# Kernel optimization log

Measured on AMD Instinct MI355X. Metric: run time of the kernel, lower is better.

## Reference

```python
import jax, jax.numpy as jnp
import numpy as np

L, H, D, DH, DFF = 6, 8, 512, 64, 2048
EPS = 1e-5


def setup_inputs() -> dict:
    key = jax.random.key(0)
    ks = jax.random.split(key, 20)
    B, S, T = 16, 512, 512
    s = 0.02
    inp = {
        "x": jax.random.normal(ks[0], (B, S, D), jnp.float32),
        "y": jax.random.normal(ks[1], (B, T, D), jnp.float32),
        # self-attention per-head projections, stacked over layers and heads
        "Wq1": jax.random.normal(ks[2], (L, H, D, DH), jnp.float32) * s,
        "Wk1": jax.random.normal(ks[3], (L, H, D, DH), jnp.float32) * s,
        "Wv1": jax.random.normal(ks[4], (L, H, D, DH), jnp.float32) * s,
        "Wo1": jax.random.normal(ks[5], (L, D, D), jnp.float32) * s,
        # cross-attention
        "Wq2": jax.random.normal(ks[6], (L, H, D, DH), jnp.float32) * s,
        "Wk2": jax.random.normal(ks[7], (L, H, D, DH), jnp.float32) * s,
        "Wv2": jax.random.normal(ks[8], (L, H, D, DH), jnp.float32) * s,
        "Wo2": jax.random.normal(ks[9], (L, D, D), jnp.float32) * s,
        # position-wise FFN
        "W1": jax.random.normal(ks[10], (L, D, DFF), jnp.float32) * s,
        "bf1": jnp.zeros((L, DFF), jnp.float32),
        "W2": jax.random.normal(ks[11], (L, DFF, D), jnp.float32) * s,
        "bf2": jnp.zeros((L, D), jnp.float32),
        # layer norms
        "ln1_g": jnp.ones((L, D), jnp.float32), "ln1_b": jnp.zeros((L, D), jnp.float32),
        "ln2_g": jnp.ones((L, D), jnp.float32), "ln2_b": jnp.zeros((L, D), jnp.float32),
        "ln3_g": jnp.ones((L, D), jnp.float32), "ln3_b": jnp.zeros((L, D), jnp.float32),
    }
    return inp


def _layer_norm(x, g, b):
    m = jnp.mean(x, axis=-1, keepdims=True)
    v = jnp.mean(jnp.square(x - m), axis=-1, keepdims=True)
    return (x - m) * jax.lax.rsqrt(v + EPS) * g + b


def _mha(q_in, kv_in, Wq, Wk, Wv, Wo, causal):
    # Wq/Wk/Wv: [H, D, DH]; batched equivalent of the per-head Linear loop
    q = jnp.einsum("bsd,hdk->bhsk", q_in, Wq)
    k = jnp.einsum("btd,hdk->bhtk", kv_in, Wk)
    v = jnp.einsum("btd,hdk->bhtk", kv_in, Wv)
    scores = jnp.einsum("bhsk,bhtk->bhst", q, k) / jnp.sqrt(jnp.float32(DH))
    if causal:
        S, T = scores.shape[-2], scores.shape[-1]
        mask = jnp.tril(jnp.ones((S, T), bool))
        scores = jnp.where(mask, scores, -jnp.inf)
    p = jax.nn.softmax(scores, axis=-1)
    out = jnp.einsum("bhst,bhtk->bhsk", p, v)
    B, _, S, _ = out.shape
    out = out.transpose(0, 2, 1, 3).reshape(B, S, H * DH)  # concat heads (dim=2 order)
    return out @ Wo


def reference(x, y, Wq1, Wk1, Wv1, Wo1, Wq2, Wk2, Wv2, Wo2,
              W1, bf1, W2, bf2, ln1_g, ln1_b, ln2_g, ln2_b, ln3_g, ln3_b):
    for l in range(L):
        # masked self-attention + residual + LN  (dropout = identity in eval)
        a1 = _mha(x, x, Wq1[l], Wk1[l], Wv1[l], Wo1[l], causal=True)
        h1 = _layer_norm(a1 + x, ln1_g[l], ln1_b[l])
        # cross-attention (queries from decoder, K/V from encoder output y)
        a2 = _mha(h1, y, Wq2[l], Wk2[l], Wv2[l], Wo2[l], causal=False)
        h2 = _layer_norm(a2 + h1, ln2_g[l], ln2_b[l])
        # position-wise FFN (batched over all positions)
        f = jax.nn.relu(h2 @ W1[l] + bf1[l]) @ W2[l] + bf2[l]
        x = _layer_norm(f + h2, ln3_g[l], ln3_b[l])
    return x
```

## Files before the change

kernel.cpp:

```cpp
#include <hip/hip_runtime.h>

typedef __bf16 bf16;
typedef __attribute__((ext_vector_type(8))) __bf16 bf16x8;
typedef __attribute__((ext_vector_type(4))) __bf16 bf16x4;
typedef __attribute__((ext_vector_type(4))) float f32x4;

#define GL16(gp, lp) __builtin_amdgcn_global_load_lds( \
    (const __attribute__((address_space(1))) unsigned int*)(gp), \
    (__attribute__((address_space(3))) unsigned int*)(lp), 16, 0, 0)

__device__ __forceinline__ f32x4 mfma16(bf16x8 a, bf16x8 b, f32x4 c) {
  return __builtin_amdgcn_mfma_f32_16x16x32_bf16(a, b, c, 0, 0, 0);
}

template<int BN, int RELU, int BIAS, int RES, int OUTB, int VTO>
__global__ __launch_bounds__(256, (BN == 64) ? 3 : 2) void gemm_k(
    const bf16* __restrict__ A, const bf16* __restrict__ Bt,
    float* __restrict__ Cf, bf16* __restrict__ Cb,
    const float* __restrict__ bias, const bf16* __restrict__ resid,
    bf16* __restrict__ vt, int vtc0,
    int M, int N, int ldc, int K)
{
  constexpr int MI = 4;
  constexpr int NI = BN / 32;
  __shared__ __align__(16) bf16 smem[(2 * 128 + 2 * BN) * 64];
  bf16* Al0 = smem;
  bf16* Bl0 = smem + 2 * 128 * 64;
  const int tid = threadIdx.x;
  const int wid = tid >> 6, lane = tid & 63;
  const int g = lane >> 4, l16 = lane & 15;

  const int lin = blockIdx.x + gridDim.x * blockIdx.y;
  const int nwg = gridDim.x * gridDim.y;
  int bx, by;
  if ((nwg & 7) == 0 && gridDim.y == 64 && gridDim.x >= 16) {
    const int xcd = lin & 7, c = lin >> 3;
    by = (xcd << 3) + (c & 7);
    bx = c >> 3;
  } else if ((nwg & 7) == 0) {
    const int l2 = (lin & 7) * (nwg >> 3) + (lin >> 3);
    bx = l2 % gridDim.x; by = l2 / gridDim.x;
  } else {
    bx = lin % gridDim.x; by = lin / gridDim.x;
  }

  const int bm = by * 128, bn = bx * BN;
  const int wm = (wid >> 1) * 64;
  const int wn = (wid & 1) * (BN / 2);

  const f32x4 z4 = {0.f, 0.f, 0.f, 0.f};
  f32x4 acc[MI][NI];
#pragma unroll
  for (int i = 0; i < MI; ++i)
#pragma unroll
    for (int j = 0; j < NI; ++j) acc[i][j] = z4;

  const int sr = tid >> 3;
  const int scs = ((((tid & 7) * 16) ^ ((sr & 7) << 4)) >> 1);
  const bf16* Ag = A + (size_t)(bm + sr) * K + scs;
  const bf16* Bg = Bt + (size_t)(bn + sr) * K + scs;
  const size_t kstep32 = (size_t)32 * K;

  auto stage = [&](int sel, int k0) {
#pragma unroll
    for (int sw = 0; sw < 4; ++sw)
      GL16(Ag + k0 + sw * kstep32, &Al0[sel * 8192 + sw * 2048 + tid * 8]);
#pragma unroll
    for (int sw = 0; sw < BN / 32; ++sw)
      GL16(Bg + k0 + sw * kstep32, &Bl0[sel * (BN * 64) + sw * 2048 + tid * 8]);
  };

  const int nsteps = K >> 6;
  stage(0, 0);
  int cur = 0;
  for (int s = 0; s < nsteps; ++s) {
    __builtin_amdgcn_sched_barrier(0);
    asm volatile("s_waitcnt vmcnt(0)" ::: "memory");
    __builtin_amdgcn_s_barrier();
    __builtin_amdgcn_sched_barrier(0);
    if (s + 1 < nsteps) stage(cur ^ 1, (s + 1) * 64);
    bf16x8 af[MI][2], bfr[NI][2];
#pragma unroll
    for (int mi = 0; mi < MI; ++mi) {
      const int row = wm + mi * 16 + l16;
      const int rs = (row & 7) << 4;
#pragma unroll
      for (int kh = 0; kh < 2; ++kh)
        af[mi][kh] = *(const bf16x8*)&Al0[cur * 8192 + row * 64 + (((g * 16 + kh * 64) ^ rs) >> 1)];
    }
#pragma unroll
    for (int ni = 0; ni < NI; ++ni) {
      const int row = wn + ni * 16 + l16;
      const int rs = (row & 7) << 4;
#pragma unroll
      for (int kh = 0; kh < 2; ++kh)
        bfr[ni][kh] = *(const bf16x8*)&Bl0[cur * (BN * 64) + row * 64 + (((g * 16 + kh * 64) ^ rs) >> 1)];
    }
#pragma unroll
    for (int kh = 0; kh < 2; ++kh)
#pragma unroll
      for (int mi = 0; mi < MI; ++mi)
#pragma unroll
        for (int ni = 0; ni < NI; ++ni)
          acc[mi][ni] = mfma16(af[mi][kh], bfr[ni][kh], acc[mi][ni]);
    cur ^= 1;
  }

  if (VTO && bn >= vtc0) {
    __syncthreads();
    bf16* stg = smem;
#pragma unroll
    for (int mi = 0; mi < MI; ++mi) {
#pragma unroll
      for (int ni = 0; ni < NI; ++ni) {
        const int dhl = wn + ni * 16 + l16;
        const int t0 = wm + mi * 16 + g * 4;
        bf16x4 v4;
#pragma unroll
        for (int r = 0; r < 4; ++r) v4[r] = (bf16)acc[mi][ni][r];
        *(bf16x4*)&stg[dhl * 136 + t0] = v4;
      }
    }
    __syncthreads();
    const int b0 = bm >> 9, tseg = bm & 511;
#pragma unroll
    for (int it = 0; it < BN / 16; ++it) {
      const int flat = it * 256 + tid;
      const int dhl = flat >> 4;
      const int t8 = (flat & 15) * 8;
      const int gdh = bn + dhl - vtc0;
      const int lL = gdh >> 9, hh = (gdh >> 6) & 7, dh = gdh & 63;
      const bf16x8 v = *(const bf16x8*)&stg[dhl * 136 + t8];
      *(bf16x8*)&vt[(((size_t)lL * 128 + b0 * 8 + hh) * 64 + dh) * 512 + tseg + t8] = v;
    }
    return;
  }

#pragma unroll
  for (int mi = 0; mi < MI; ++mi) {
#pragma unroll
    for (int ni = 0; ni < NI; ++ni) {
#pragma unroll
      for (int r = 0; r < 4; ++r) {
        const int row = bm + wm + mi * 16 + g * 4 + r;
        const int col = bn + wn + ni * 16 + l16;
        float v = acc[mi][ni][r];
        if (BIAS) v += bias[col];
        const size_t idx = (size_t)row * ldc + col;
        if (RES)  v += (float)resid[idx];
        if (RELU) v = fmaxf(v, 0.f);
        if (OUTB) Cb[idx] = (bf16)v;
        else      Cf[idx] = v;
      }
    }
  }
}

template<int CAUSAL>
__global__ __launch_bounds__(256, 4) void attn_k(
    const bf16* __restrict__ Q, const bf16* __restrict__ Kg,
    const bf16* __restrict__ VT, bf16* __restrict__ O, int qs, int kvs)
{
  __shared__ __align__(16) bf16 Kl[2][64 * 64];
  __shared__ __align__(16) bf16 Vl[2][64 * 64];
  __shared__ __align__(16) bf16 plb[4 * 16 * 64];
  const int tid = threadIdx.x;
  const int wid = tid >> 6, lane = tid & 63;
  const int g = lane >> 4, l16 = lane & 15;

  int lin = blockIdx.x + 8 * blockIdx.y + 64 * blockIdx.z;
  lin = (lin & 7) * 128 + (lin >> 3);
  const int qt = lin & 7, h = (lin >> 3) & 7, b = lin >> 6;

  const int q0 = qt * 64 + wid * 16;
  const size_t tokQ = (size_t)b * 512 + q0;

  const bf16* qp = Q + (tokQ + l16) * (size_t)qs + h * 64 + g * 8;
  const bf16x8 qf0 = *(const bf16x8*)qp;
  const bf16x8 qf1 = *(const bf16x8*)(qp + 32);

  const int sr = tid >> 3;
  const int cs2 = ((((tid & 7) * 16) ^ ((sr & 7) << 4)) >> 1);
  const bf16* Ksrc = Kg + ((size_t)b * 512 + sr) * kvs + h * 64 + cs2;
  const bf16* Vsrc = VT + (size_t)(b * 8 + h) * 64 * 512 + (size_t)sr * 512 + cs2;
  bf16* pw = plb + wid * 1024;

  auto stage = [&](int sel, int t0) {
    GL16(Ksrc + (size_t)t0 * kvs, &Kl[sel][tid * 8]);
    GL16(Ksrc + (size_t)(t0 + 32) * kvs, &Kl[sel][tid * 8 + 2048]);
    GL16(Vsrc + t0, &Vl[sel][tid * 8]);
    GL16(Vsrc + 32 * 512 + t0, &Vl[sel][tid * 8 + 2048]);
  };

  const f32x4 z4 = {0.f, 0.f, 0.f, 0.f};
  float m[4], ls[4];
  f32x4 o[4];
#pragma unroll
  for (int r = 0; r < 4; ++r) { m[r] = -1e30f; ls[r] = 0.f; o[r] = z4; }

  const int sw = (l16 & 7) << 4;
  const int ktmax = CAUSAL ? qt : 7;
  stage(0, 0);
  int cur = 0;
  for (int kt = 0; kt <= ktmax; ++kt) {
    const int t0 = kt * 64;
    __builtin_amdgcn_sched_barrier(0);
    asm volatile("s_waitcnt vmcnt(0)" ::: "memory");
    __builtin_amdgcn_s_barrier();
    if (kt < ktmax) stage(cur ^ 1, t0 + 64);

    f32x4 sc[4];
#pragma unroll
    for (int jt = 0; jt < 4; ++jt) {
      const int rk = jt * 16 + l16;
      const bf16x8 kf0 = *(const bf16x8*)&Kl[cur][rk * 64 + (((g * 16) ^ sw) >> 1)];
      const bf16x8 kf1 = *(const bf16x8*)&Kl[cur][rk * 64 + (((g * 16 + 64) ^ sw) >> 1)];
      sc[jt] = mfma16(qf0, kf0, z4);
      sc[jt] = mfma16(qf1, kf1, sc[jt]);
    }
#pragma unroll
    for (int r = 0; r < 4; ++r) {
      const int q = g * 4 + r;
      const int srow = q0 + q;
      const int qs7 = (q & 7) << 4;
      float pv[4];
      float mx = -1e30f;
#pragma unroll
      for (int jt = 0; jt < 4; ++jt) {
        float v = sc[jt][r] * 0.125f;
        if (CAUSAL && (t0 + jt * 16 + l16) > srow) v = -1e30f;
        pv[jt] = v;
        mx = fmaxf(mx, v);
      }
#pragma unroll
      for (int msk = 8; msk; msk >>= 1) mx = fmaxf(mx, __shfl_xor(mx, msk));
      const float mn = fmaxf(m[r], mx);
      const float corr = __expf(m[r] - mn);
      float s = 0.f;
#pragma unroll
      for (int jt = 0; jt < 4; ++jt) {
        const float p = __expf(pv[jt] - mn);
        s += p;
        const int sb = (((jt * 16 + l16) * 2) ^ qs7) >> 1;
        pw[q * 64 + sb] = (bf16)p;
      }
#pragma unroll
      for (int msk = 8; msk; msk >>= 1) s += __shfl_xor(s, msk);
      ls[r] = ls[r] * corr + s;
      m[r] = mn;
#pragma unroll
      for (int j = 0; j < 4; ++j) o[j][r] *= corr;
    }
    asm volatile("s_waitcnt lgkmcnt(0)" ::: "memory");
    __builtin_amdgcn_sched_barrier(0);
    const bf16x8 pa0 = *(const bf16x8*)&pw[l16 * 64 + (((g * 16) ^ sw) >> 1)];
    const bf16x8 pa1 = *(const bf16x8*)&pw[l16 * 64 + (((g * 16 + 64) ^ sw) >> 1)];
#pragma unroll
    for (int j = 0; j < 4; ++j) {
      const int rv = j * 16 + l16;
      const bf16x8 vf0 = *(const bf16x8*)&Vl[cur][rv * 64 + (((g * 16) ^ sw) >> 1)];
      const bf16x8 vf1 = *(const bf16x8*)&Vl[cur][rv * 64 + (((g * 16 + 64) ^ sw) >> 1)];
      o[j] = mfma16(pa0, vf0, o[j]);
      o[j] = mfma16(pa1, vf1, o[j]);
    }
    cur ^= 1;
  }
#pragma unroll
  for (int r = 0; r < 4; ++r) {
    const float inv = 1.f / ls[r];
    bf16* op = O + (tokQ + g * 4 + r) * 512 + h * 64;
#pragma unroll
    for (int j = 0; j < 4; ++j) op[j * 16 + l16] = (bf16)(o[j][r] * inv);
  }
}

__global__ __launch_bounds__(256) void ln_k(
    const float* __restrict__ z, const float* __restrict__ gam,
    const float* __restrict__ bet, float* __restrict__ of,
    bf16* __restrict__ ob)
{
  const int wid = threadIdx.x >> 6, lane = threadIdx.x & 63;
  const int row = blockIdx.x * 4 + wid;
  const f32x4* zr = (const f32x4*)(z + (size_t)row * 512);
  const f32x4 a = zr[lane], c = zr[lane + 64];
  float s = 0.f, ss = 0.f;
#pragma unroll
  for (int e = 0; e < 4; ++e) {
    s += a[e] + c[e];
    ss += a[e] * a[e] + c[e] * c[e];
  }
#pragma unroll
  for (int msk = 32; msk; msk >>= 1) {
    s += __shfl_xor(s, msk);
    ss += __shfl_xor(ss, msk);
  }
  const float mean = s * (1.f / 512.f);
  const float var = ss * (1.f / 512.f) - mean * mean;
  const float rstd = rsqrtf(var + 1e-5f);
  const f32x4* gp = (const f32x4*)gam;
  const f32x4* bp = (const f32x4*)bet;
  const f32x4 g0 = gp[lane], g1 = gp[lane + 64];
  const f32x4 b0 = bp[lane], b1 = bp[lane + 64];
  f32x4 o0, o1;
#pragma unroll
  for (int e = 0; e < 4; ++e) {
    o0[e] = (a[e] - mean) * rstd * g0[e] + b0[e];
    o1[e] = (c[e] - mean) * rstd * g1[e] + b1[e];
  }
  if (of) {
    f32x4* ofr = (f32x4*)(of + (size_t)row * 512);
    ofr[lane] = o0;
    ofr[lane + 64] = o1;
  }
  if (ob) {
    bf16x4 c0, c1;
#pragma unroll
    for (int e = 0; e < 4; ++e) { c0[e] = (bf16)o0[e]; c1[e] = (bf16)o1[e]; }
    bf16x4* obr = (bf16x4*)(ob + (size_t)row * 512);
    obr[lane] = c0;
    obr[lane + 64] = c1;
  }
}

__global__ void transpose_cast(const float* __restrict__ src, bf16* __restrict__ dst,
                               int R, int C, int bpl, size_t lstride, size_t boff)
{
  __shared__ float t[32][33];
  const int z = blockIdx.z;
  src += (size_t)z * R * C;
  dst += (size_t)(z / bpl) * lstride + (size_t)(z % bpl) * ((size_t)R * C) + boff;
  const int c0 = blockIdx.x * 32, r0 = blockIdx.y * 32;
  const int tx = threadIdx.x, ty = threadIdx.y;
#pragma unroll
  for (int j = 0; j < 32; j += 8)
    t[ty + j][tx] = src[(size_t)(r0 + ty + j) * C + c0 + tx];
  __syncthreads();
#pragma unroll
  for (int j = 0; j < 32; j += 8)
    dst[(size_t)(c0 + ty + j) * R + r0 + tx] = (bf16)t[tx][ty + j];
}

__global__ void cast4(const float* __restrict__ s, bf16* __restrict__ d)
{
  const int i = blockIdx.x * 256 + threadIdx.x;
  const f32x4 v = ((const f32x4*)s)[i];
  bf16x4 c;
#pragma unroll
  for (int e = 0; e < 4; ++e) c[e] = (bf16)v[e];
  ((bf16x4*)d)[i] = c;
}

extern "C" void kernel_launch(void* const* d_in, const int* in_sizes, int n_in,
                              void* d_out, int out_size, void* d_ws, size_t ws_size,
                              hipStream_t stream)
{
  (void)in_sizes; (void)n_in; (void)out_size; (void)ws_size;
  const float* x   = (const float*)d_in[0];
  const float* y   = (const float*)d_in[1];
  const float* Wq1 = (const float*)d_in[2];
  const float* Wk1 = (const float*)d_in[3];
  const float* Wv1 = (const float*)d_in[4];
  const float* Wo1 = (const float*)d_in[5];
  const float* Wq2 = (const float*)d_in[6];
  const float* Wk2 = (const float*)d_in[7];
  const float* Wv2 = (const float*)d_in[8];
  const float* Wo2 = (const float*)d_in[9];
  const float* W1  = (const float*)d_in[10];
  const float* b1  = (const float*)d_in[11];
  const float* W2  = (const float*)d_in[12];
  const float* b2  = (const float*)d_in[13];
  const float* ln1g = (const float*)d_in[14];
  const float* ln1b = (const float*)d_in[15];
  const float* ln2g = (const float*)d_in[16];
  const float* ln2b = (const float*)d_in[17];
  const float* ln3g = (const float*)d_in[18];
  const float* ln3b = (const float*)d_in[19];

  char* ws = (char*)d_ws;
  size_t off = 0;
  auto alloc = [&](size_t bytes) -> void* {
    void* p = (void*)(ws + off);
    off += (bytes + 255) & ~(size_t)255;
    return p;
  };

  bf16* wqkv1t = (bf16*)alloc((size_t)6 * 1536 * 512 * 2);
  bf16* wo1t   = (bf16*)alloc((size_t)6 * 512 * 512 * 2);
  bf16* wq2t   = (bf16*)alloc((size_t)6 * 512 * 512 * 2);
  bf16* wkv2t  = (bf16*)alloc((size_t)6144 * 512 * 2);
  bf16* wo2t   = (bf16*)alloc((size_t)6 * 512 * 512 * 2);
  bf16* w1t    = (bf16*)alloc((size_t)6 * 512 * 2048 * 2);
  bf16* w2t    = (bf16*)alloc((size_t)6 * 2048 * 512 * 2);
  bf16* xb   = (bf16*)alloc((size_t)8192 * 512 * 2);
  bf16* yb   = (bf16*)alloc((size_t)8192 * 512 * 2);
  bf16* qkvb = (bf16*)alloc((size_t)8192 * 1536 * 2);
  bf16* qb   = (bf16*)alloc((size_t)8192 * 512 * 2);
  bf16* ab   = (bf16*)alloc((size_t)8192 * 512 * 2);
  bf16* h1b  = (bf16*)alloc((size_t)8192 * 512 * 2);
  bf16* h2b  = (bf16*)alloc((size_t)8192 * 512 * 2);
  float* zf  = (float*)alloc((size_t)8192 * 512 * 4);
  bf16* vt1  = (bf16*)alloc((size_t)8192 * 512 * 2);
  bf16* k2all  = (bf16*)alloc((size_t)8192 * 3072 * 2);
  bf16* vt2all = (bf16*)alloc((size_t)6 * 8192 * 512 * 2);
  bf16* f1b  = qkvb;

  const dim3 tb(32, 8);
  transpose_cast<<<dim3(2, 16, 48), tb, 0, stream>>>(Wq1, wqkv1t, 512, 64, 8, (size_t)1536 * 512, 0);
  transpose_cast<<<dim3(2, 16, 48), tb, 0, stream>>>(Wk1, wqkv1t, 512, 64, 8, (size_t)1536 * 512, (size_t)512 * 512);
  transpose_cast<<<dim3(2, 16, 48), tb, 0, stream>>>(Wv1, wqkv1t, 512, 64, 8, (size_t)1536 * 512, (size_t)1024 * 512);
  transpose_cast<<<dim3(16, 16, 6), tb, 0, stream>>>(Wo1, wo1t, 512, 512, 1, (size_t)512 * 512, 0);
  transpose_cast<<<dim3(2, 16, 48), tb, 0, stream>>>(Wq2, wq2t, 512, 64, 8, (size_t)512 * 512, 0);
  transpose_cast<<<dim3(2, 16, 48), tb, 0, stream>>>(Wk2, wkv2t, 512, 64, 8, (size_t)512 * 512, 0);
  transpose_cast<<<dim3(2, 16, 48), tb, 0, stream>>>(Wv2, wkv2t + (size_t)3072 * 512, 512, 64, 8, (size_t)512 * 512, 0);
  transpose_cast<<<dim3(16, 16, 6), tb, 0, stream>>>(Wo2, wo2t, 512, 512, 1, (size_t)512 * 512, 0);
  transpose_cast<<<dim3(64, 16, 6), tb, 0, stream>>>(W1, w1t, 512, 2048, 1, (size_t)512 * 2048, 0);
  transpose_cast<<<dim3(16, 64, 6), tb, 0, stream>>>(W2, w2t, 2048, 512, 1, (size_t)2048 * 512, 0);
  cast4<<<4096, 256, 0, stream>>>(x, xb);
  cast4<<<4096, 256, 0, stream>>>(y, yb);

  const dim3 g512s(8, 64), g1536(12, 64), gff(16, 64), g6144(48, 64);

  gemm_k<128, 0, 0, 0, 1, 1><<<g6144, 256, 0, stream>>>(yb, wkv2t, nullptr, k2all,
                                                        nullptr, nullptr, vt2all, 3072,
                                                        8192, 6144, 3072, 512);

  const bf16* curxb = xb;
  for (int l = 0; l < 6; ++l) {
    const bf16* WQKV1 = wqkv1t + (size_t)l * 1536 * 512;
    const bf16* WO1   = wo1t   + (size_t)l * 512 * 512;
    const bf16* WQ2   = wq2t   + (size_t)l * 512 * 512;
    const bf16* WO2   = wo2t   + (size_t)l * 512 * 512;
    const bf16* W1T   = w1t    + (size_t)l * 2048 * 512;
    const bf16* W2T   = w2t    + (size_t)l * 512 * 2048;

    gemm_k<128, 0, 0, 0, 1, 1><<<g1536, 256, 0, stream>>>(curxb, WQKV1, nullptr, qkvb,
                                                          nullptr, nullptr, vt1, 1024,
                                                          8192, 1536, 1536, 512);
    attn_k<1><<<dim3(8, 8, 16), 256, 0, stream>>>(qkvb, qkvb + 512, vt1, ab, 1536, 1536);
    gemm_k<64, 0, 0, 1, 0, 0><<<g512s, 256, 0, stream>>>(ab, WO1, zf, nullptr,
                                                         nullptr, curxb, nullptr, 0,
                                                         8192, 512, 512, 512);
    ln_k<<<2048, 256, 0, stream>>>(zf, ln1g + l * 512, ln1b + l * 512, nullptr, h1b);

    gemm_k<64, 0, 0, 0, 1, 0><<<g512s, 256, 0, stream>>>(h1b, WQ2, nullptr, qb,
                                                         nullptr, nullptr, nullptr, 0,
                                                         8192, 512, 512, 512);
    attn_k<0><<<dim3(8, 8, 16), 256, 0, stream>>>(qb, k2all + (size_t)l * 512,
                                                  vt2all + (size_t)l * 8192 * 512, ab, 512, 3072);
    gemm_k<64, 0, 0, 1, 0, 0><<<g512s, 256, 0, stream>>>(ab, WO2, zf, nullptr,
                                                         nullptr, h1b, nullptr, 0,
                                                         8192, 512, 512, 512);
    ln_k<<<2048, 256, 0, stream>>>(zf, ln2g + l * 512, ln2b + l * 512, nullptr, h2b);

    gemm_k<128, 1, 1, 0, 1, 0><<<gff, 256, 0, stream>>>(h2b, W1T, nullptr, f1b,
                                                        b1 + l * 2048, nullptr, nullptr, 0,
                                                        8192, 2048, 2048, 512);
    gemm_k<64, 0, 1, 1, 0, 0><<<g512s, 256, 0, stream>>>(f1b, W2T, zf, nullptr,
                                                         b2 + l * 512, h2b, nullptr, 0,
                                                         8192, 512, 512, 2048);
    float* outf = (l == 5) ? (float*)d_out : nullptr;
    bf16* outb  = (l == 5) ? nullptr : xb;
    ln_k<<<2048, 256, 0, stream>>>(zf, ln3g + l * 512, ln3b + l * 512, outf, outb);
    curxb = xb;
  }
}
```

Measured before the change: 1.134 ms.

## Split-K the FFN down-projection GEMM and raise wave priority around attention MFMAs

The W2 GEMM (K=2048) is split into two K halves via blockIdx.z, writing separate fp32 partials that the following layernorm kernel sums. Bias and residual are added only in the first split. This doubles the number of workgroups so the GPU is better occupied, at the cost of an extra fp32 partial buffer write and read. The attention kernel also sets a higher wave priority around its MFMA blocks. The partial buffer reuses the attention output allocation, which must be large enough to hold fp32 data.

```diff
diff --git a/kernel.cpp b/kernel.cpp
--- a/kernel.cpp
+++ b/kernel.cpp
@@ -16,10 +16,10 @@
 template<int BN, int RELU, int BIAS, int RES, int OUTB, int VTO>
 __global__ __launch_bounds__(256, (BN == 64) ? 3 : 2) void gemm_k(
     const bf16* __restrict__ A, const bf16* __restrict__ Bt,
-    float* __restrict__ Cf, bf16* __restrict__ Cb,
+    float* __restrict__ Cf, float* __restrict__ Cf2, bf16* __restrict__ Cb,
     const float* __restrict__ bias, const bf16* __restrict__ resid,
     bf16* __restrict__ vt, int vtc0,
-    int M, int N, int ldc, int K)
+    int M, int N, int ldc, int K, int lda)
 {
   constexpr int MI = 4;
   constexpr int NI = BN / 32;
@@ -29,6 +29,11 @@
   const int tid = threadIdx.x;
   const int wid = tid >> 6, lane = tid & 63;
   const int g = lane >> 4, l16 = lane & 15;
+
+  const int kz = blockIdx.z;
+  A += (size_t)kz * K;
+  Bt += (size_t)kz * K;
+  if (kz) Cf = Cf2;
 
   const int lin = blockIdx.x + gridDim.x * blockIdx.y;
   const int nwg = gridDim.x * gridDim.y;
@@ -57,9 +62,9 @@
 
   const int sr = tid >> 3;
   const int scs = ((((tid & 7) * 16) ^ ((sr & 7) << 4)) >> 1);
-  const bf16* Ag = A + (size_t)(bm + sr) * K + scs;
-  const bf16* Bg = Bt + (size_t)(bn + sr) * K + scs;
-  const size_t kstep32 = (size_t)32 * K;
+  const bf16* Ag = A + (size_t)(bm + sr) * lda + scs;
+  const bf16* Bg = Bt + (size_t)(bn + sr) * lda + scs;
+  const size_t kstep32 = (size_t)32 * lda;
 
   auto stage = [&](int sel, int k0) {
 #pragma unroll
@@ -145,9 +150,9 @@
         const int row = bm + wm + mi * 16 + g * 4 + r;
         const int col = bn + wn + ni * 16 + l16;
         float v = acc[mi][ni][r];
-        if (BIAS) v += bias[col];
+        if (BIAS && kz == 0) v += bias[col];
         const size_t idx = (size_t)row * ldc + col;
-        if (RES)  v += (float)resid[idx];
+        if (RES && kz == 0)  v += (float)resid[idx];
         if (RELU) v = fmaxf(v, 0.f);
         if (OUTB) Cb[idx] = (bf16)v;
         else      Cf[idx] = v;
@@ -210,6 +215,7 @@
     if (kt < ktmax) stage(cur ^ 1, t0 + 64);
 
     f32x4 sc[4];
+    __builtin_amdgcn_s_setprio(1);
 #pragma unroll
     for (int jt = 0; jt < 4; ++jt) {
       const int rk = jt * 16 + l16;
@@ -218,6 +224,7 @@
       sc[jt] = mfma16(qf0, kf0, z4);
       sc[jt] = mfma16(qf1, kf1, sc[jt]);
     }
+    __builtin_amdgcn_s_setprio(0);
 #pragma unroll
     for (int r = 0; r < 4; ++r) {
       const int q = g * 4 + r;
@@ -255,6 +262,7 @@
     __builtin_amdgcn_sched_barrier(0);
     const bf16x8 pa0 = *(const bf16x8*)&pw[l16 * 64 + (((g * 16) ^ sw) >> 1)];
     const bf16x8 pa1 = *(const bf16x8*)&pw[l16 * 64 + (((g * 16 + 64) ^ sw) >> 1)];
+    __builtin_amdgcn_s_setprio(1);
 #pragma unroll
     for (int j = 0; j < 4; ++j) {
       const int rv = j * 16 + l16;
@@ -263,6 +271,7 @@
       o[j] = mfma16(pa0, vf0, o[j]);
       o[j] = mfma16(pa1, vf1, o[j]);
     }
+    __builtin_amdgcn_s_setprio(0);
     cur ^= 1;
   }
 #pragma unroll
@@ -275,14 +284,20 @@
 }
 
 __global__ __launch_bounds__(256) void ln_k(
-    const float* __restrict__ z, const float* __restrict__ gam,
-    const float* __restrict__ bet, float* __restrict__ of,
-    bf16* __restrict__ ob)
+    const float* __restrict__ z, const float* __restrict__ z2,
+    const float* __restrict__ gam, const float* __restrict__ bet,
+    float* __restrict__ of, bf16* __restrict__ ob)
 {
   const int wid = threadIdx.x >> 6, lane = threadIdx.x & 63;
   const int row = blockIdx.x * 4 + wid;
   const f32x4* zr = (const f32x4*)(z + (size_t)row * 512);
-  const f32x4 a = zr[lane], c = zr[lane + 64];
+  f32x4 a = zr[lane], c = zr[lane + 64];
+  if (z2) {
+    const f32x4* z2r = (const f32x4*)(z2 + (size_t)row * 512);
+    const f32x4 a2 = z2r[lane], c2 = z2r[lane + 64];
+#pragma unroll
+    for (int e = 0; e < 4; ++e) { a[e] += a2[e]; c[e] += c2[e]; }
+  }
   float s = 0.f, ss = 0.f;
 #pragma unroll
   for (int e = 0; e < 4; ++e) {
@@ -403,6 +418,7 @@
   bf16* k2all  = (bf16*)alloc((size_t)8192 * 3072 * 2);
   bf16* vt2all = (bf16*)alloc((size_t)6 * 8192 * 512 * 2);
   bf16* f1b  = qkvb;
+  float* zf2 = (float*)ab;
 
   const dim3 tb(32, 8);
   transpose_cast<<<dim3(2, 16, 48), tb, 0, stream>>>(Wq1, wqkv1t, 512, 64, 8, (size_t)1536 * 512, 0);
@@ -419,10 +435,11 @@
   cast4<<<4096, 256, 0, stream>>>(y, yb);
 
   const dim3 g512s(8, 64), g1536(12, 64), gff(16, 64), g6144(48, 64);
-
-  gemm_k<128, 0, 0, 0, 1, 1><<<g6144, 256, 0, stream>>>(yb, wkv2t, nullptr, k2all,
+  const dim3 gW2(8, 64, 2);
+
+  gemm_k<128, 0, 0, 0, 1, 1><<<g6144, 256, 0, stream>>>(yb, wkv2t, nullptr, nullptr, k2all,
                                                         nullptr, nullptr, vt2all, 3072,
-                                                        8192, 6144, 3072, 512);
+                                                        8192, 6144, 3072, 512, 512);
 
   const bf16* curxb = xb;
   for (int l = 0; l < 6; ++l) {
@@ -433,34 +450,34 @@
     const bf16* W1T   = w1t    + (size_t)l * 2048 * 512;
     const bf16* W2T   = w2t    + (size_t)l * 512 * 2048;
 
-    gemm_k<128, 0, 0, 0, 1, 1><<<g1536, 256, 0, stream>>>(curxb, WQKV1, nullptr, qkvb,
+    gemm_k<128, 0, 0, 0, 1, 1><<<g1536, 256, 0, stream>>>(curxb, WQKV1, nullptr, nullptr, qkvb,
                                                           nullptr, nullptr, vt1, 1024,
-                                                          8192, 1536, 1536, 512);
+                                                          8192, 1536, 1536, 512, 512);
     attn_k<1><<<dim3(8, 8, 16), 256, 0, stream>>>(qkvb, qkvb + 512, vt1, ab, 1536, 1536);
-    gemm_k<64, 0, 0, 1, 0, 0><<<g512s, 256, 0, stream>>>(ab, WO1, zf, nullptr,
+    gemm_k<64, 0, 0, 1, 0, 0><<<g512s, 256, 0, stream>>>(ab, WO1, zf, nullptr, nullptr,
                                                          nullptr, curxb, nullptr, 0,
-                                                         8192, 512, 512, 512);
-    ln_k<<<2048, 256, 0, stream>>>(zf, ln1g + l * 512, ln1b + l * 512, nullptr, h1b);
-
-    gemm_k<64, 0, 0, 0, 1, 0><<<g512s, 256, 0, stream>>>(h1b, WQ2, nullptr, qb,
+                                                         8192, 512, 512, 512, 512);
+    ln_k<<<2048, 256, 0, stream>>>(zf, nullptr, ln1g + l * 512, ln1b + l * 512, nullptr, h1b);
+
+    gemm_k<64, 0, 0, 0, 1, 0><<<g512s, 256, 0, stream>>>(h1b, WQ2, nullptr, nullptr, qb,
                                                          nullptr, nullptr, nullptr, 0,
-                                                         8192, 512, 512, 512);
+                                                         8192, 512, 512, 512, 512);
     attn_k<0><<<dim3(8, 8, 16), 256, 0, stream>>>(qb, k2all + (size_t)l * 512,
                                                   vt2all + (size_t)l * 8192 * 512, ab, 512, 3072);
-    gemm_k<64, 0, 0, 1, 0, 0><<<g512s, 256, 0, stream>>>(ab, WO2, zf, nullptr,
+    gemm_k<64, 0, 0, 1, 0, 0><<<g512s, 256, 0, stream>>>(ab, WO2, zf, nullptr, nullptr,
                                                          nullptr, h1b, nullptr, 0,
-                                                         8192, 512, 512, 512);
-    ln_k<<<2048, 256, 0, stream>>>(zf, ln2g + l * 512, ln2b + l * 512, nullptr, h2b);
-
-    gemm_k<128, 1, 1, 0, 1, 0><<<gff, 256, 0, stream>>>(h2b, W1T, nullptr, f1b,
+                                                         8192, 512, 512, 512, 512);
+    ln_k<<<2048, 256, 0, stream>>>(zf, nullptr, ln2g + l * 512, ln2b + l * 512, nullptr, h2b);
+
+    gemm_k<128, 1, 1, 0, 1, 0><<<gff, 256, 0, stream>>>(h2b, W1T, nullptr, nullptr, f1b,
                                                         b1 + l * 2048, nullptr, nullptr, 0,
-                                                        8192, 2048, 2048, 512);
-    gemm_k<64, 0, 1, 1, 0, 0><<<g512s, 256, 0, stream>>>(f1b, W2T, zf, nullptr,
-                                                         b2 + l * 512, h2b, nullptr, 0,
-                                                         8192, 512, 512, 2048);
+                                                        8192, 2048, 2048, 512, 512);
+    gemm_k<64, 0, 1, 1, 0, 0><<<gW2, 256, 0, stream>>>(f1b, W2T, zf, zf2, nullptr,
+                                                       b2 + l * 512, h2b, nullptr, 0,
+                                                       8192, 512, 512, 1024, 2048);
     float* outf = (l == 5) ? (float*)d_out : nullptr;
     bf16* outb  = (l == 5) ? nullptr : xb;
-    ln_k<<<2048, 256, 0, stream>>>(zf, ln3g + l * 512, ln3b + l * 512, outf, outb);
+    ln_k<<<2048, 256, 0, stream>>>(zf, zf2, ln3g + l * 512, ln3b + l * 512, outf, outb);
     curxb = xb;
   }
 }
```

Result: slower. 1.335 ms (+17.8%).
